# Kernel optimization log

Measured on AMD Instinct MI355X. Metric: run time of the kernel, lower is better.

## Reference

```python
import jax, jax.numpy as jnp
import numpy as np

HID = 11  # int(np.sqrt(128))
EMB = 128
NUM_VAR = 1000

def setup_inputs() -> dict:
    key = jax.random.key(0)
    k1, k2, k3, k4, k5, k6 = jax.random.split(key, 6)
    value = jax.random.normal(k1, (4096, 200), dtype=jnp.float32)
    var_id = jax.random.randint(k2, (4096, 200), 0, NUM_VAR + 1, dtype=jnp.int32)
    category_mask = jax.random.randint(k3, (4096, 200), 0, 2, dtype=jnp.int32)
    # glorot-uniform-like params
    W1 = jax.random.uniform(k4, (1, HID), jnp.float32, -1.0, 1.0) * np.sqrt(6.0 / (1 + HID))
    b1 = jnp.zeros((HID,), jnp.float32)
    W2 = jax.random.uniform(k5, (HID, EMB), jnp.float32, -1.0, 1.0) * np.sqrt(6.0 / (HID + EMB))
    emb_table = jax.random.uniform(k6, (NUM_VAR + 1, EMB), jnp.float32, -0.05, 0.05)
    return {"value": value, "var_id": var_id, "category_mask": category_mask,
            "W1": W1, "b1": b1, "W2": W2, "emb_table": emb_table}

def reference(value, var_id, category_mask, W1, b1, W2, emb_table):
    # CVE: per-scalar tiny MLP 1 -> HID -> EMB
    h = jnp.tanh(value[..., None] * W1[0] + b1)          # [B, L, HID]
    values_emb = jnp.einsum('blh,he->ble', h, W2)         # [B, L, EMB]
    values_emb = values_emb * category_mask.astype(jnp.float32)[..., None]
    var_id_emb = emb_table[var_id]                        # gather [B, L, EMB]
    sum_emb = values_emb + var_id_emb
    padding_mask = jnp.clip(var_id.astype(jnp.float32), 0.0, 1.0)
    return sum_emb, padding_mask
```

## Files before the change

### kernel.cpp

```cpp
#include <hip/hip_runtime.h>
#include <hip/hip_bf16.h>

#define EMB 128
#define HID 11
#define UNROLL 4

typedef float f32x4 __attribute__((ext_vector_type(4)));

__device__ __forceinline__ float fast_tanh(float x) {
    float ax = fabsf(x);
    float e  = __expf(2.0f * ax);
    float r  = 1.0f - 2.0f * __builtin_amdgcn_rcpf(e + 1.0f);
    return copysignf(r, x);
}

__global__ __launch_bounds__(256, 2) void tabenc_kernel(
    const float* __restrict__ value,
    const int*   __restrict__ var_id,
    const int*   __restrict__ cmask,
    const float* __restrict__ W1,
    const float* __restrict__ b1,
    const float* __restrict__ W2,
    const float* __restrict__ emb,
    float*       __restrict__ out_sum,
    float*       __restrict__ out_pm,
    int n_tokens)
{
    const int tid  = threadIdx.x;
    const int lane = tid & 63;
    const int half = lane >> 5;
    const int sub  = lane & 31;
    const int sb   = lane & 32;
    const int c0   = sub << 2;

    f32x4 w2[HID];
#pragma unroll
    for (int h = 0; h < HID; ++h)
        w2[h] = *reinterpret_cast<const f32x4*>(W2 + h * EMB + c0);

    float w1v = 0.0f, b1v = 0.0f;
    if (sub < HID) { w1v = W1[sub]; b1v = b1[sub]; }

    const int gwave  = (blockIdx.x << 2) + (tid >> 6);
    const int nwaves = gridDim.x << 2;
    const int nwU    = nwaves * UNROLL;
    const int npair  = (n_tokens + 1) >> 1;
    const int tmax   = n_tokens - 1;

    for (int w = gwave; w < npair; w += nwU) {
        int   tok[UNROLL];
        bool  act[UNROLL];
        float v[UNROLL];
        int   id[UNROLL];
        float fm[UNROLL];

#pragma unroll
        for (int k = 0; k < UNROLL; ++k) {
            const int wk = w + k * nwaves;
            act[k] = (wk < npair);
            int t = 2 * wk + half;
            if (t > tmax) t = tmax;
            tok[k] = t;
            v[k]  = value[t];
            id[k] = var_id[t];
            fm[k] = (float)cmask[t];
        }

        f32x4 e[UNROLL];
#pragma unroll
        for (int k = 0; k < UNROLL; ++k)
            e[k] = *reinterpret_cast<const f32x4*>(emb + (long)id[k] * EMB + c0);

        float hv[UNROLL];
#pragma unroll
        for (int k = 0; k < UNROLL; ++k)
            hv[k] = fast_tanh(fmaf(v[k], w1v, b1v));

        f32x4 acc[UNROLL];
#pragma unroll
        for (int k = 0; k < UNROLL; ++k)
            acc[k] = (f32x4){0.f, 0.f, 0.f, 0.f};

#pragma unroll
        for (int hh = 0; hh < HID; ++hh) {
#pragma unroll
            for (int k = 0; k < UNROLL; ++k) {
                const float kk = __shfl(hv[k], sb + hh, 64);
                acc[k] += kk * w2[hh];
            }
        }

#pragma unroll
        for (int k = 0; k < UNROLL; ++k) {
            if (!act[k]) continue;
            const f32x4 o = acc[k] * fm[k] + e[k];
            __builtin_nontemporal_store(o,
                reinterpret_cast<f32x4*>(out_sum + (long)tok[k] * EMB + c0));
            if (sub == 0)
                out_pm[tok[k]] = (id[k] > 0) ? 1.0f : 0.0f;
        }
    }
}

extern "C" void kernel_launch(void* const* d_in, const int* in_sizes, int n_in,
                              void* d_out, int out_size, void* d_ws, size_t ws_size,
                              hipStream_t stream) {
    const float* value  = (const float*)d_in[0];
    const int*   var_id = (const int*)  d_in[1];
    const int*   cmask  = (const int*)  d_in[2];
    const float* W1     = (const float*)d_in[3];
    const float* b1     = (const float*)d_in[4];
    const float* W2     = (const float*)d_in[5];
    const float* emb    = (const float*)d_in[6];

    const int n_tokens = in_sizes[0];
    float* out_sum = (float*)d_out;
    float* out_pm  = (float*)d_out + (long long)n_tokens * EMB;

    const int waves_needed  = (n_tokens + 1) / 2;
    const int blocks_needed = (waves_needed + 3) / 4;
    const int grid = blocks_needed < 2048 ? blocks_needed : 2048;

    tabenc_kernel<<<grid, 256, 0, stream>>>(value, var_id, cmask, W1, b1, W2,
                                            emb, out_sum, out_pm, n_tokens);
}
```

Before: 97.75 us.

## Software-pipeline token loads one iteration ahead with two pairs per step

Replaces the 4-way unrolled batch with a double-buffered loop that processes two token pairs per iteration. The next iteration's value, id, mask and embedding-row loads are issued before the current MLP compute and stores, so memory latency can overlap with compute. Fewer independent loads are in flight per iteration in exchange for cross-iteration overlap, and some register pressure is added by holding both buffers. On the last iteration the loads are clamped but unused.

```diff
diff --git a/kernel.cpp b/kernel.cpp
--- a/kernel.cpp
+++ b/kernel.cpp
@@ -3,7 +3,7 @@
 
 #define EMB 128
 #define HID 11
-#define UNROLL 4
+#define PAIRS 2
 
 typedef float f32x4 __attribute__((ext_vector_type(4)));
 
@@ -43,20 +43,22 @@
 
     const int gwave  = (blockIdx.x << 2) + (tid >> 6);
     const int nwaves = gridDim.x << 2;
-    const int nwU    = nwaves * UNROLL;
+    const int nwS    = nwaves * PAIRS;
     const int npair  = (n_tokens + 1) >> 1;
     const int tmax   = n_tokens - 1;
 
-    for (int w = gwave; w < npair; w += nwU) {
-        int   tok[UNROLL];
-        bool  act[UNROLL];
-        float v[UNROLL];
-        int   id[UNROLL];
-        float fm[UNROLL];
+    if (gwave >= npair) return;
 
+    int   tokC[PAIRS]; bool actC[PAIRS]; float vC[PAIRS];
+    int   idC[PAIRS];  float fmC[PAIRS];  f32x4 eC[PAIRS];
+    int   tokN[PAIRS]; bool actN[PAIRS]; float vN[PAIRS];
+    int   idN[PAIRS];  float fmN[PAIRS];  f32x4 eN[PAIRS];
+
+    auto LOAD = [&](int wbase, int* tok, bool* act, float* v, int* id,
+                    float* fm, f32x4* e) {
 #pragma unroll
-        for (int k = 0; k < UNROLL; ++k) {
-            const int wk = w + k * nwaves;
+        for (int k = 0; k < PAIRS; ++k) {
+            const int wk = wbase + k * nwaves;
             act[k] = (wk < npair);
             int t = 2 * wk + half;
             if (t > tmax) t = tmax;
@@ -65,39 +67,50 @@
             id[k] = var_id[t];
             fm[k] = (float)cmask[t];
         }
+#pragma unroll
+        for (int k = 0; k < PAIRS; ++k)
+            e[k] = *reinterpret_cast<const f32x4*>(emb + (long)id[k] * EMB + c0);
+    };
 
-        f32x4 e[UNROLL];
+    LOAD(gwave, tokC, actC, vC, idC, fmC, eC);
+
+    for (int w = gwave; w < npair; w += nwS) {
+        LOAD(w + nwS, tokN, actN, vN, idN, fmN, eN);
+
+        float hv[PAIRS];
 #pragma unroll
-        for (int k = 0; k < UNROLL; ++k)
-            e[k] = *reinterpret_cast<const f32x4*>(emb + (long)id[k] * EMB + c0);
+        for (int k = 0; k < PAIRS; ++k)
+            hv[k] = fast_tanh(fmaf(vC[k], w1v, b1v));
 
-        float hv[UNROLL];
+        f32x4 acc[PAIRS];
 #pragma unroll
-        for (int k = 0; k < UNROLL; ++k)
-            hv[k] = fast_tanh(fmaf(v[k], w1v, b1v));
-
-        f32x4 acc[UNROLL];
-#pragma unroll
-        for (int k = 0; k < UNROLL; ++k)
+        for (int k = 0; k < PAIRS; ++k)
             acc[k] = (f32x4){0.f, 0.f, 0.f, 0.f};
 
 #pragma unroll
         for (int hh = 0; hh < HID; ++hh) {
 #pragma unroll
-            for (int k = 0; k < UNROLL; ++k) {
+            for (int k = 0; k < PAIRS; ++k) {
                 const float kk = __shfl(hv[k], sb + hh, 64);
                 acc[k] += kk * w2[hh];
             }
         }
 
 #pragma unroll
-        for (int k = 0; k < UNROLL; ++k) {
-            if (!act[k]) continue;
-            const f32x4 o = acc[k] * fm[k] + e[k];
-            __builtin_nontemporal_store(o,
-                reinterpret_cast<f32x4*>(out_sum + (long)tok[k] * EMB + c0));
-            if (sub == 0)
-                out_pm[tok[k]] = (id[k] > 0) ? 1.0f : 0.0f;
+        for (int k = 0; k < PAIRS; ++k) {
+            if (actC[k]) {
+                const f32x4 o = acc[k] * fmC[k] + eC[k];
+                __builtin_nontemporal_store(o,
+                    reinterpret_cast<f32x4*>(out_sum + (long)tokC[k] * EMB + c0));
+                if (sub == 0)
+                    out_pm[tokC[k]] = (idC[k] > 0) ? 1.0f : 0.0f;
+            }
+        }
+
+#pragma unroll
+        for (int k = 0; k < PAIRS; ++k) {
+            tokC[k] = tokN[k]; actC[k] = actN[k]; vC[k] = vN[k];
+            idC[k]  = idN[k];  fmC[k]  = fmN[k];  eC[k] = eN[k];
         }
     }
 }
```

New measurement: 95.45 us. 2.4% less time.
